# Optimization experiments

Measured on AMD Instinct MI355X. Metric: run time of the kernel, lower is better.

The kernel has to match this reference:

```python
import jax, jax.numpy as jnp
import numpy as np
import math

NUM_HEADS = 2


def setup_inputs() -> dict:
    key = jax.random.key(0)
    k1, k2, k3, k4 = jax.random.split(key, 4)
    B, S, E = 16, 2048, 8  # embed_dim == n_wires == 8 (required by module structure)
    x = jax.random.normal(k1, (B, S, E), dtype=jnp.float32)
    theta = jax.random.normal(k2, (E,), dtype=jnp.float32)          # trainable RX angles, one per wire
    w_out = jax.random.normal(k3, (E, E), dtype=jnp.float32) / math.sqrt(E)  # out_proj weight
    b_out = jax.random.normal(k4, (E,), dtype=jnp.float32) * 0.01   # out_proj bias
    return {"x": x, "theta": theta, "w_out": w_out, "b_out": b_out}


def reference(x, theta, w_out, b_out):
    B, S, E = x.shape
    H = NUM_HEADS
    dk = E // H
    # Quantum projection, analytic form: per-wire RX(x) then RX(theta) on |0>,
    # PauliZ expectation -> cos(x + theta). Same layer applied for q, k, v.
    q = jnp.cos(x + theta)              # [B, S, E]
    qh = q.reshape(B, S, H, dk).transpose(0, 2, 1, 3)  # [B, H, S, dk]; q == k == v
    scores = jnp.einsum('bhqd,bhkd->bhqk', qh, qh) / jnp.sqrt(jnp.float32(dk))
    attn = jax.nn.softmax(scores, axis=-1)             # dropout is identity in eval
    out = jnp.einsum('bhqk,bhkd->bhqd', attn, qh)      # [B, H, S, dk]
    out = out.transpose(0, 2, 1, 3).reshape(B, S, E)
    return out @ w_out.T + b_out
```

## Files before the change

kernel.cpp:

```cpp
#include <hip/hip_runtime.h>
#include <math.h>

#define BB 16
#define SS 2048
#define HH 2
#define RPB 128
#define THREADS 1024
#define KHALF (SS / 2)
#define NITER (KHALF / 16)
#define KVT_STRIDE 2064

typedef _Float16 half8 __attribute__((ext_vector_type(8)));
typedef _Float16 half4h __attribute__((ext_vector_type(4)));
typedef _Float16 half2h __attribute__((ext_vector_type(2)));
typedef float floatx4 __attribute__((ext_vector_type(4)));

__device__ __forceinline__ float fast_exp2(float x) {
  return __builtin_amdgcn_exp2f(x);
}
__device__ __forceinline__ half2h pkrtz(float a, float b) {
  return __builtin_bit_cast(half2h, __builtin_amdgcn_cvt_pkrtz(a, b));
}

__global__ __launch_bounds__(THREADS, 8)
void qattn_fused(const float* __restrict__ x,
                 const float* __restrict__ theta,
                 const float* __restrict__ w_out,
                 const float* __restrict__ b_out,
                 float* __restrict__ out) {
  __shared__ half8 s_keys[SS];
  __shared__ _Float16 s_kvT[5 * KVT_STRIDE];
  __shared__ float po[RPB * 2 * 5];

  const int bid = blockIdx.x;
  const int rb  = bid & 15;
  const int h   = (bid >> 4) & 1;
  const int b   = bid >> 5;
  const int t   = threadIdx.x;

  const float4 th = ((const float4*)theta)[h];
  const float4* xb = (const float4*)x;

  for (int s = t; s < SS; s += THREADS) {
    float4 xr = xb[(size_t)(b * SS + s) * 2 + h];
    float c0 = __cosf(xr.x + th.x), c1 = __cosf(xr.y + th.y);
    float c2 = __cosf(xr.z + th.z), c3 = __cosf(xr.w + th.w);
    const _Float16 z = (_Float16)0.0f;
    half8 v = {(_Float16)c0, (_Float16)c1, (_Float16)c2, (_Float16)c3, z, z, z, z};
    s_keys[s] = v;
    s_kvT[0 * KVT_STRIDE + s] = (_Float16)c0;
    s_kvT[1 * KVT_STRIDE + s] = (_Float16)c1;
    s_kvT[2 * KVT_STRIDE + s] = (_Float16)c2;
    s_kvT[3 * KVT_STRIDE + s] = (_Float16)c3;
  }
  for (int i = t; i < KVT_STRIDE; i += THREADS)
    s_kvT[4 * KVT_STRIDE + i] = (_Float16)1.0f;
  __syncthreads();

  const int lane = t & 63;
  const int wv   = t >> 6;
  const int tile = wv >> 1;
  const int hf   = wv & 1;
  const int quad = lane >> 4;
  const int l15  = lane & 15;

  const float KS  = 0.72134752044448170367f;
  const float scl = (lane < 16) ? KS : 0.0f;
  half4h rq = *(const half4h*)&s_keys[rb * RPB + tile * 16 + l15];
  const _Float16 z = (_Float16)0.0f;
  half8 bq = {(_Float16)((float)rq[0] * scl), (_Float16)((float)rq[1] * scl),
              (_Float16)((float)rq[2] * scl), (_Float16)((float)rq[3] * scl),
              z, z, z, z};

  const _Float16* bb = s_kvT + (l15 < 4 ? l15 : 4) * KVT_STRIDE + hf * KHALF + quad * 4;
  const half8* ak = s_keys + hf * KHALF;

  floatx4 o = {0.f, 0.f, 0.f, 0.f};
  const floatx4 zf = {0.f, 0.f, 0.f, 0.f};

#pragma unroll 2
  for (int kt = 0; kt < NITER; ++kt) {
    half8 a = ak[kt * 16 + l15];
    half4h bl = *(const half4h*)(bb + kt * 16);
    half8 bpv = {bl[0], bl[1], bl[2], bl[3], z, z, z, z};

    floatx4 c = __builtin_amdgcn_mfma_f32_16x16x32_f16(a, bq, zf, 0, 0, 0);

    half2h p01 = pkrtz(fast_exp2(c[0]), fast_exp2(c[1]));
    half2h p23 = pkrtz(fast_exp2(c[2]), fast_exp2(c[3]));
    half8 apv = {p01[0], p01[1], p23[0], p23[1], z, z, z, z};

    o = __builtin_amdgcn_mfma_f32_16x16x32_f16(apv, bpv, o, 0, 0, 0);
  }

  if (l15 < 5) {
#pragma unroll
    for (int r = 0; r < 4; ++r)
      po[((tile * 16 + quad * 4 + r) * 2 + hf) * 5 + l15] = o[r];
  }
  __syncthreads();

  {
    const int row = t >> 3;
    const int e   = t & 7;
    const float* pr = po + row * 10;
    const float n0 = pr[0] + pr[5];
    const float n1 = pr[1] + pr[6];
    const float n2 = pr[2] + pr[7];
    const float n3 = pr[3] + pr[8];
    const float inv = 1.0f / (pr[4] + pr[9]);
    const float* wr = w_out + e * 8 + h * 4;
    float val = fmaf(n0, wr[0], fmaf(n1, wr[1], fmaf(n2, wr[2], n3 * wr[3]))) * inv;
    if (h == 0) val += b_out[e];
    atomicAdd(out + ((size_t)(b * SS + rb * RPB + row)) * 8 + e, val);
  }
}

extern "C" void kernel_launch(void* const* d_in, const int* in_sizes, int n_in,
                              void* d_out, int out_size, void* d_ws, size_t ws_size,
                              hipStream_t stream) {
  const float* x     = (const float*)d_in[0];
  const float* theta = (const float*)d_in[1];
  const float* w_out = (const float*)d_in[2];
  const float* b_out = (const float*)d_in[3];
  float* out = (float*)d_out;
  (void)in_sizes; (void)n_in; (void)d_ws; (void)ws_size;

  (void)hipMemsetAsync(d_out, 0, (size_t)out_size * sizeof(float), stream);
  qattn_fused<<<dim3(BB * HH * 16), THREADS, 0, stream>>>(x, theta, w_out, b_out, out);
}
```

Measured before the change: 80.54 us.

## Replace exact softmax attention with truncated Taylor/Chebyshev linear-attention expansion

Replaces the O(S^2) MFMA attention with a polynomial feature expansion: exp(q·k/sqrt(dk)) is approximated by a degree-7 Chebyshev/Bessel series in monomials of the cosine features. Key-side moment sums are accumulated per (batch, head) in a first kernel, and a second kernel contracts them with each query's monomials, then applies the output projection. This removes quadratic work but is only an approximation, accurate because |q·k|/2 ≤ 2 for cosine inputs bounded by 1. The truncation error may or may not meet tolerance.

```diff
diff --git a/kernel.cpp b/kernel.cpp
--- a/kernel.cpp
+++ b/kernel.cpp
@@ -3,116 +3,201 @@
 
 #define BB 16
 #define SS 2048
-#define HH 2
-#define RPB 128
-#define THREADS 1024
-#define KHALF (SS / 2)
-#define NITER (KHALF / 16)
-#define KVT_STRIDE 2064
-
-typedef _Float16 half8 __attribute__((ext_vector_type(8)));
-typedef _Float16 half4h __attribute__((ext_vector_type(4)));
-typedef _Float16 half2h __attribute__((ext_vector_type(2)));
-typedef float floatx4 __attribute__((ext_vector_type(4)));
-
-__device__ __forceinline__ float fast_exp2(float x) {
-  return __builtin_amdgcn_exp2f(x);
-}
-__device__ __forceinline__ half2h pkrtz(float a, float b) {
-  return __builtin_bit_cast(half2h, __builtin_amdgcn_cvt_pkrtz(a, b));
-}
-
-__global__ __launch_bounds__(THREADS, 8)
-void qattn_fused(const float* __restrict__ x,
-                 const float* __restrict__ theta,
-                 const float* __restrict__ w_out,
-                 const float* __restrict__ b_out,
-                 float* __restrict__ out) {
-  __shared__ half8 s_keys[SS];
-  __shared__ _Float16 s_kvT[5 * KVT_STRIDE];
-  __shared__ float po[RPB * 2 * 5];
-
-  const int bid = blockIdx.x;
-  const int rb  = bid & 15;
-  const int h   = (bid >> 4) & 1;
-  const int b   = bid >> 5;
-  const int t   = threadIdx.x;
-
+#define NF 330
+#define NS 495
+#define SPAD 512
+#define NTILE 31
+
+struct E4 { unsigned char e0, e1, e2, e3; };
+
+struct Tables {
+  E4 se[496];
+  E4 fe[330];
+  float fc[330];
+  short sidx[330][5];
+};
+
+constexpr int T1c(int n){ return n+1; }
+constexpr int T2c(int n){ return (n+1)*(n+2)/2; }
+constexpr int T3c(int n){ return (n+1)*(n+2)*(n+3)/6; }
+constexpr int rank8(int a,int b,int c,int d){
+  int r = 0;
+  for (int e0=0;e0<a;++e0) r += T3c(8-e0);
+  for (int e1=0;e1<b;++e1) r += T2c(8-a-e1);
+  for (int e2=0;e2<c;++e2) r += T1c(8-a-b-e2);
+  return r + d;
+}
+constexpr double besselI2(int n){
+  double t = 1.0;
+  for (int i=1;i<=n;++i) t /= (double)i;
+  double s = 0.0;
+  for (int m=0;m<14;++m){ if (m>0) t /= (double)(m*(m+n)); s += t; }
+  return s;
+}
+constexpr Tables gen(){
+  Tables T{};
+  double cheb[8] = {};
+  for (int n=0;n<8;++n) cheb[n] = (n==0?1.0:2.0)*besselI2(n);
+  const int tm[8][8] = {
+    {1,0,0,0,0,0,0,0},{0,1,0,0,0,0,0,0},{-1,0,2,0,0,0,0,0},{0,-3,0,4,0,0,0,0},
+    {1,0,-8,0,8,0,0,0},{0,5,0,-20,0,16,0,0},{-1,0,18,0,-48,0,32,0},{0,-7,0,56,0,-112,0,64}};
+  double bk[8] = {};
+  double p2 = 1.0;
+  for (int k=0;k<8;++k){
+    double tc = 0.0;
+    for (int n=0;n<8;++n) tc += cheb[n]*(double)tm[n][k];
+    bk[k] = tc/p2;
+    p2 *= 2.0;
+  }
+  const double fact[9] = {1,1,2,6,24,120,720,5040,40320};
+  {
+    int idx = 0;
+    for (int a=0;a<=8;++a) for (int b=0;b<=8-a;++b) for (int c=0;c<=8-a-b;++c)
+      for (int d=0;d<=8-a-b-c;++d){
+        T.se[idx].e0=(unsigned char)a; T.se[idx].e1=(unsigned char)b;
+        T.se[idx].e2=(unsigned char)c; T.se[idx].e3=(unsigned char)d; ++idx;
+      }
+  }
+  {
+    int idx = 0;
+    for (int a=0;a<=7;++a) for (int b=0;b<=7-a;++b) for (int c=0;c<=7-a-b;++c)
+      for (int d=0;d<=7-a-b-c;++d){
+        const int k = a+b+c+d;
+        const double mult = fact[k]/(fact[a]*fact[b]*fact[c]*fact[d]);
+        double pk = 1.0; for (int i=0;i<k;++i) pk *= 2.0;
+        T.fe[idx].e0=(unsigned char)a; T.fe[idx].e1=(unsigned char)b;
+        T.fe[idx].e2=(unsigned char)c; T.fe[idx].e3=(unsigned char)d;
+        T.fc[idx] = (float)(bk[k]*mult/pk);
+        T.sidx[idx][0] = (short)rank8(a+1,b,c,d);
+        T.sidx[idx][1] = (short)rank8(a,b+1,c,d);
+        T.sidx[idx][2] = (short)rank8(a,b,c+1,d);
+        T.sidx[idx][3] = (short)rank8(a,b,c,d+1);
+        T.sidx[idx][4] = (short)rank8(a,b,c,d);
+        ++idx;
+      }
+  }
+  return T;
+}
+constexpr Tables TAB = gen();
+
+template<int T>
+__device__ __forceinline__ void sum_tile(const float4* __restrict__ x4,
+                                         float4 th, int b, int h, int t,
+                                         float* __restrict__ wsbh){
+  float acc[16];
+#pragma unroll
+  for (int i=0;i<16;++i) acc[i] = 0.f;
+  for (int rr=0; rr<8; ++rr){
+    const int s = (rr<<8) + t;
+    float4 xr = x4[(size_t)(b*SS+s)*2 + h];
+    const float q0 = __cosf(xr.x + th.x), q1 = __cosf(xr.y + th.y),
+                q2 = __cosf(xr.z + th.z), q3 = __cosf(xr.w + th.w);
+    float p0[9], p1[9], p2[9], p3[9];
+    p0[0]=1.f; p1[0]=1.f; p2[0]=1.f; p3[0]=1.f;
+#pragma unroll
+    for (int e=1;e<9;++e){
+      p0[e]=p0[e-1]*q0; p1[e]=p1[e-1]*q1; p2[e]=p2[e-1]*q2; p3[e]=p3[e-1]*q3;
+    }
+#pragma unroll
+    for (int i=0;i<16;++i){
+      if (T*16+i < NS){
+        const E4 e = TAB.se[T*16+i];
+        acc[i] += p0[e.e0]*p1[e.e1]*p2[e.e2]*p3[e.e3];
+      }
+    }
+  }
+  const int lane = (int)(threadIdx.x & 63);
+#pragma unroll
+  for (int i=0;i<16;++i){
+    if (T*16+i < NS){
+      float v = acc[i];
+#pragma unroll
+      for (int st=1; st<64; st<<=1) v += __shfl_xor(v, st, 64);
+      if (lane == 0) atomicAdd(wsbh + T*16 + i, v);
+    }
+  }
+}
+
+__global__ __launch_bounds__(256)
+void qsum_kernel(const float* __restrict__ x, const float* __restrict__ theta,
+                 float* __restrict__ ws){
+  const int tile = blockIdx.x & 31;
+  if (tile >= NTILE) return;
+  const int bh = blockIdx.x >> 5;
+  const int b = bh >> 1, h = bh & 1;
+  const int t = (int)threadIdx.x;
   const float4 th = ((const float4*)theta)[h];
-  const float4* xb = (const float4*)x;
-
-  for (int s = t; s < SS; s += THREADS) {
-    float4 xr = xb[(size_t)(b * SS + s) * 2 + h];
-    float c0 = __cosf(xr.x + th.x), c1 = __cosf(xr.y + th.y);
-    float c2 = __cosf(xr.z + th.z), c3 = __cosf(xr.w + th.w);
-    const _Float16 z = (_Float16)0.0f;
-    half8 v = {(_Float16)c0, (_Float16)c1, (_Float16)c2, (_Float16)c3, z, z, z, z};
-    s_keys[s] = v;
-    s_kvT[0 * KVT_STRIDE + s] = (_Float16)c0;
-    s_kvT[1 * KVT_STRIDE + s] = (_Float16)c1;
-    s_kvT[2 * KVT_STRIDE + s] = (_Float16)c2;
-    s_kvT[3 * KVT_STRIDE + s] = (_Float16)c3;
-  }
-  for (int i = t; i < KVT_STRIDE; i += THREADS)
-    s_kvT[4 * KVT_STRIDE + i] = (_Float16)1.0f;
+  const float4* x4 = (const float4*)x;
+  float* wsbh = ws + (size_t)bh * SPAD;
+  switch(tile){
+#define KCASE(n) case n: sum_tile<n>(x4, th, b, h, t, wsbh); break;
+    KCASE(0) KCASE(1) KCASE(2) KCASE(3) KCASE(4) KCASE(5) KCASE(6) KCASE(7)
+    KCASE(8) KCASE(9) KCASE(10) KCASE(11) KCASE(12) KCASE(13) KCASE(14) KCASE(15)
+    KCASE(16) KCASE(17) KCASE(18) KCASE(19) KCASE(20) KCASE(21) KCASE(22) KCASE(23)
+    KCASE(24) KCASE(25) KCASE(26) KCASE(27) KCASE(28) KCASE(29) KCASE(30)
+#undef KCASE
+  }
+}
+
+__global__ __launch_bounds__(256)
+void qout_kernel(const float* __restrict__ x, const float* __restrict__ theta,
+                 const float* __restrict__ ws, const float* __restrict__ w_out,
+                 const float* __restrict__ b_out, float* __restrict__ out){
+  __shared__ float po[128 * 8];
+  const int t   = (int)threadIdx.x;
+  const int blk = (int)blockIdx.x;
+  const int b   = blk >> 4;
+  const int s0  = (blk & 15) << 7;
+  const int lane = t & 63;
+  const int h  = __builtin_amdgcn_readfirstlane((t >> 6) & 1);
+  const int rr = ((t >> 7) << 6) | lane;
+  const int s  = s0 + rr;
+
+  const float4 th = ((const float4*)theta)[h];
+  float4 xr = ((const float4*)x)[(size_t)(b*SS+s)*2 + h];
+  const float q0 = __cosf(xr.x + th.x), q1 = __cosf(xr.y + th.y),
+              q2 = __cosf(xr.z + th.z), q3 = __cosf(xr.w + th.w);
+  float p0[8], p1[8], p2[8], p3[8];
+  p0[0]=1.f; p1[0]=1.f; p2[0]=1.f; p3[0]=1.f;
+#pragma unroll
+  for (int e=1;e<8;++e){
+    p0[e]=p0[e-1]*q0; p1[e]=p1[e-1]*q1; p2[e]=p2[e-1]*q2; p3[e]=p3[e-1]*q3;
+  }
+  const float* Sp = ws + (size_t)((b<<1) + h) * SPAD;
+  float n0=0.f, n1=0.f, n2=0.f, n3=0.f, dn=0.f;
+#pragma unroll
+  for (int F=0; F<NF; ++F){
+    const E4 e = TAB.fe[F];
+    const float m = p0[e.e0]*p1[e.e1]*p2[e.e2]*p3[e.e3]*TAB.fc[F];
+    n0 = fmaf(m, Sp[TAB.sidx[F][0]], n0);
+    n1 = fmaf(m, Sp[TAB.sidx[F][1]], n1);
+    n2 = fmaf(m, Sp[TAB.sidx[F][2]], n2);
+    n3 = fmaf(m, Sp[TAB.sidx[F][3]], n3);
+    dn = fmaf(m, Sp[TAB.sidx[F][4]], dn);
+  }
+  const float inv = 1.0f / dn;
+  po[rr*8 + h*4 + 0] = n0*inv;
+  po[rr*8 + h*4 + 1] = n1*inv;
+  po[rr*8 + h*4 + 2] = n2*inv;
+  po[rr*8 + h*4 + 3] = n3*inv;
   __syncthreads();
 
-  const int lane = t & 63;
-  const int wv   = t >> 6;
-  const int tile = wv >> 1;
-  const int hf   = wv & 1;
-  const int quad = lane >> 4;
-  const int l15  = lane & 15;
-
-  const float KS  = 0.72134752044448170367f;
-  const float scl = (lane < 16) ? KS : 0.0f;
-  half4h rq = *(const half4h*)&s_keys[rb * RPB + tile * 16 + l15];
-  const _Float16 z = (_Float16)0.0f;
-  half8 bq = {(_Float16)((float)rq[0] * scl), (_Float16)((float)rq[1] * scl),
-              (_Float16)((float)rq[2] * scl), (_Float16)((float)rq[3] * scl),
-              z, z, z, z};
-
-  const _Float16* bb = s_kvT + (l15 < 4 ? l15 : 4) * KVT_STRIDE + hf * KHALF + quad * 4;
-  const half8* ak = s_keys + hf * KHALF;
-
-  floatx4 o = {0.f, 0.f, 0.f, 0.f};
-  const floatx4 zf = {0.f, 0.f, 0.f, 0.f};
-
-#pragma unroll 2
-  for (int kt = 0; kt < NITER; ++kt) {
-    half8 a = ak[kt * 16 + l15];
-    half4h bl = *(const half4h*)(bb + kt * 16);
-    half8 bpv = {bl[0], bl[1], bl[2], bl[3], z, z, z, z};
-
-    floatx4 c = __builtin_amdgcn_mfma_f32_16x16x32_f16(a, bq, zf, 0, 0, 0);
-
-    half2h p01 = pkrtz(fast_exp2(c[0]), fast_exp2(c[1]));
-    half2h p23 = pkrtz(fast_exp2(c[2]), fast_exp2(c[3]));
-    half8 apv = {p01[0], p01[1], p23[0], p23[1], z, z, z, z};
-
-    o = __builtin_amdgcn_mfma_f32_16x16x32_f16(apv, bpv, o, 0, 0, 0);
-  }
-
-  if (l15 < 5) {
-#pragma unroll
-    for (int r = 0; r < 4; ++r)
-      po[((tile * 16 + quad * 4 + r) * 2 + hf) * 5 + l15] = o[r];
-  }
-  __syncthreads();
-
-  {
-    const int row = t >> 3;
-    const int e   = t & 7;
-    const float* pr = po + row * 10;
-    const float n0 = pr[0] + pr[5];
-    const float n1 = pr[1] + pr[6];
-    const float n2 = pr[2] + pr[7];
-    const float n3 = pr[3] + pr[8];
-    const float inv = 1.0f / (pr[4] + pr[9]);
-    const float* wr = w_out + e * 8 + h * 4;
-    float val = fmaf(n0, wr[0], fmaf(n1, wr[1], fmaf(n2, wr[2], n3 * wr[3]))) * inv;
-    if (h == 0) val += b_out[e];
-    atomicAdd(out + ((size_t)(b * SS + rb * RPB + row)) * 8 + e, val);
+  if (t < 128){
+    const float* pr = po + t*8;
+    float o[8];
+#pragma unroll
+    for (int j=0;j<8;++j) o[j] = pr[j];
+    float r[8];
+#pragma unroll
+    for (int e=0;e<8;++e){
+      float acc = b_out[e];
+#pragma unroll
+      for (int j=0;j<8;++j) acc = fmaf(o[j], w_out[e*8+j], acc);
+      r[e] = acc;
+    }
+    float* op = out + ((size_t)(b*SS + s0 + t)) * 8;
+    *(float4*)op       = make_float4(r[0], r[1], r[2], r[3]);
+    *(float4*)(op + 4) = make_float4(r[4], r[5], r[6], r[7]);
   }
 }
 
@@ -124,8 +209,10 @@
   const float* w_out = (const float*)d_in[2];
   const float* b_out = (const float*)d_in[3];
   float* out = (float*)d_out;
-  (void)in_sizes; (void)n_in; (void)d_ws; (void)ws_size;
-
-  (void)hipMemsetAsync(d_out, 0, (size_t)out_size * sizeof(float), stream);
-  qattn_fused<<<dim3(BB * HH * 16), THREADS, 0, stream>>>(x, theta, w_out, b_out, out);
-}
+  (void)in_sizes; (void)n_in; (void)out_size; (void)ws_size;
+
+  (void)hipMemsetAsync(d_ws, 0, (size_t)32 * SPAD * sizeof(float), stream);
+  qsum_kernel<<<dim3(32 * 32), 256, 0, stream>>>(x, theta, (float*)d_ws);
+  qout_kernel<<<dim3(BB * 16), 256, 0, stream>>>(x, theta, (const float*)d_ws,
+                                                 w_out, b_out, out);
+}
```

Result: slower. 88.90 us (+10.4%).
